# Performance work log

Measured on AMD Instinct MI355X. Metric: run time of the kernel, lower is better.

The kernel has to match this reference:

```python
import jax, jax.numpy as jnp
import numpy as np

DIM = 192
HEADS = 6
HEAD_DIM = DIM // HEADS          # 32
WIN = (4, 4, 4)
SHIFT = (2, 2, 2)
VOL = (64, 64, 64)               # D, H, W
N = WIN[0] * WIN[1] * WIN[2]     # 64 tokens per window
SCALE = HEAD_DIM ** -0.5
EPS = 1e-5


def _rel_pos_index():
    # static (N, N) int index into the relative-position-bias table
    w = WIN
    coords = np.stack(np.meshgrid(np.arange(w[0]), np.arange(w[1]), np.arange(w[2]), indexing='ij'))
    cf = coords.reshape(3, -1)                       # (3, N)
    rel = (cf[:, :, None] - cf[:, None, :]).transpose(1, 2, 0).astype(np.int64)  # (N, N, 3)
    rel[:, :, 0] += w[0] - 1
    rel[:, :, 1] += w[1] - 1
    rel[:, :, 2] += w[2] - 1
    rel[:, :, 0] *= (2 * w[1] - 1) * (2 * w[2] - 1)
    rel[:, :, 1] *= (2 * w[2] - 1)
    return rel.sum(-1)                               # (N, N)

REL_IDX = _rel_pos_index()


def _window_partition(x):
    # (B, D, H, W, C) -> (B*nW, N, C)
    B, D, H, W, C = x.shape
    x = x.reshape(B, D // WIN[0], WIN[0], H // WIN[1], WIN[1], W // WIN[2], WIN[2], C)
    return x.transpose(0, 1, 3, 5, 2, 4, 6, 7).reshape(-1, N, C)


def _window_reverse(windows, B, D, H, W):
    # (B*nW, N, C) -> (B, D, H, W, C)
    C = windows.shape[-1]
    x = windows.reshape(B, D // WIN[0], H // WIN[1], W // WIN[2], WIN[0], WIN[1], WIN[2], C)
    return x.transpose(0, 1, 4, 2, 5, 3, 6, 7).reshape(B, D, H, W, C)


def _layernorm(x, g, b):
    m = jnp.mean(x, axis=-1, keepdims=True)
    v = jnp.var(x, axis=-1, keepdims=True)
    return (x - m) * jax.lax.rsqrt(v + EPS) * g + b


def _compute_shift_mask():
    # Swin3D compute_mask: (nW, N, N) with 0 / -100
    Dp, Hp, Wp = VOL
    img = np.zeros((1, Dp, Hp, Wp, 1), np.float32)
    cnt = 0
    seg = lambda w, s: (slice(0, -w), slice(-w, -s), slice(-s, None))
    for d in seg(WIN[0], SHIFT[0]):
        for h in seg(WIN[1], SHIFT[1]):
            for w in seg(WIN[2], SHIFT[2]):
                img[:, d, h, w, :] = cnt
                cnt += 1
    mw = img.reshape(1, Dp // WIN[0], WIN[0], Hp // WIN[1], WIN[1], Wp // WIN[2], WIN[2], 1)
    mw = mw.transpose(0, 1, 3, 5, 2, 4, 6, 7).reshape(-1, N)   # (nW, N)
    am = mw[:, None, :] - mw[:, :, None]                        # (nW, N, N)
    return np.where(am != 0, np.float32(-100.0), np.float32(0.0))


def setup_inputs() -> dict:
    key = jax.random.key(0)
    ks = jax.random.split(key, 12)
    B = 1
    D, H, W = VOL
    p = lambda k, shape, s=0.02: (jax.random.normal(k, shape, jnp.float32) * s)
    return {
        'x': jax.random.normal(ks[0], (B, D, H, W, DIM), jnp.float32),
        'mask': jnp.asarray(_compute_shift_mask()),
        'norm1_g': jnp.ones((DIM,), jnp.float32),
        'norm1_b': jnp.zeros((DIM,), jnp.float32),
        'qkv_w': p(ks[1], (3 * DIM, DIM)),
        'qkv_b': jnp.zeros((3 * DIM,), jnp.float32),
        'rpb_table': p(ks[2], ((2 * WIN[0] - 1) * (2 * WIN[1] - 1) * (2 * WIN[2] - 1), HEADS)),
        'proj_w': p(ks[3], (DIM, DIM)),
        'proj_b': jnp.zeros((DIM,), jnp.float32),
        'norm2_g': jnp.ones((DIM,), jnp.float32),
        'norm2_b': jnp.zeros((DIM,), jnp.float32),
        'fc1_w': p(ks[4], (4 * DIM, DIM)),
        'fc1_b': jnp.zeros((4 * DIM,), jnp.float32),
        'fc2_w': p(ks[5], (DIM, 4 * DIM)),
        'fc2_b': jnp.zeros((DIM,), jnp.float32),
    }


def reference(x, mask, norm1_g, norm1_b, qkv_w, qkv_b, rpb_table, proj_w, proj_b,
              norm2_g, norm2_b, fc1_w, fc1_b, fc2_w, fc2_b):
    B, D, H, W, C = x.shape
    shortcut = x
    # --- part1: norm1 -> shift -> windowed attention -> unshift ---
    h_ = _layernorm(x, norm1_g, norm1_b)
    h_ = jnp.roll(h_, shift=(-SHIFT[0], -SHIFT[1], -SHIFT[2]), axis=(1, 2, 3))
    xw = _window_partition(h_)                                  # (B*nW, N, C)
    Bn = xw.shape[0]
    qkv = (xw @ qkv_w.T + qkv_b).reshape(Bn, N, 3, HEADS, HEAD_DIM)
    qkv = qkv.transpose(2, 0, 3, 1, 4)                          # (3, Bn, h, N, hd)
    q, k, v = qkv[0] * SCALE, qkv[1], qkv[2]
    attn = jnp.einsum('bhnd,bhmd->bhnm', q, k)                  # (Bn, h, N, N)
    bias = rpb_table[REL_IDX.reshape(-1)].reshape(N, N, HEADS).transpose(2, 0, 1)
    attn = attn + bias[None]
    nW = mask.shape[0]
    attn = attn.reshape(Bn // nW, nW, HEADS, N, N) + mask[None, :, None]
    attn = jax.nn.softmax(attn.reshape(Bn, HEADS, N, N), axis=-1)
    out = jnp.einsum('bhnm,bhmd->bhnd', attn, v).transpose(0, 2, 1, 3).reshape(Bn, N, C)
    out = out @ proj_w.T + proj_b
    h_ = _window_reverse(out, B, D, H, W)
    h_ = jnp.roll(h_, shift=SHIFT, axis=(1, 2, 3))
    x = shortcut + h_                                           # drop_path = identity
    # --- part2: norm2 -> MLP ---
    y = _layernorm(x, norm2_g, norm2_b)
    y = jax.nn.gelu(y @ fc1_w.T + fc1_b, approximate=False) @ fc2_w.T + fc2_b
    return x + y
```

## Files before the change

kernel.cpp:

```cpp
#include <hip/hip_runtime.h>

#define AS1 __attribute__((address_space(1)))
#define AS3 __attribute__((address_space(3)))

typedef short short8 __attribute__((ext_vector_type(8)));
typedef float floatx4 __attribute__((ext_vector_type(4)));

#define NTOK 262144
#define NWIN 4096
#define QKV_SCALE 0.17677669529663687f

__device__ __forceinline__ unsigned short f2bf(float f) {
  unsigned u = __builtin_bit_cast(unsigned, f);
  u += 0x7fffu + ((u >> 16) & 1u);
  return (unsigned short)(u >> 16);
}

__device__ __forceinline__ void gl_lds16(const void* g, void* l) {
  __builtin_amdgcn_global_load_lds((AS1 void*)g, (AS3 void*)l, 16, 0, 0);
}

template <int K>
__device__ __forceinline__ void gemm_core(const unsigned short* __restrict__ A,
                                          const unsigned short* __restrict__ W,
                                          int m0, int n0,
                                          unsigned short* smA, unsigned short* smB,
                                          floatx4 acc[2][4]) {
  const int t = threadIdx.x;
  const int lane = t & 63;
  const int w = t >> 6;
  const int kg = lane >> 4;
  const int l15 = lane & 15;
  const int rA = t >> 2;
  const int q = t & 3;

#pragma unroll
  for (int i = 0; i < 2; i++)
#pragma unroll
    for (int j = 0; j < 4; j++) acc[i][j] = floatx4{0.f, 0.f, 0.f, 0.f};

  for (int k0 = 0; k0 < K; k0 += 32) {
    __syncthreads();
    {
      const int s0 = (q ^ ((rA >> 1) & 3)) << 3;
      gl_lds16(A + (m0 + rA) * K + k0 + s0, (char*)smA + t * 16);
      const int r1 = rA + 64;
      const int s1 = (q ^ ((r1 >> 1) & 3)) << 3;
      gl_lds16(A + (m0 + r1) * K + k0 + s1, (char*)smA + 4096 + t * 16);
      gl_lds16(W + (n0 + rA) * K + k0 + s0, (char*)smB + t * 16);
    }
    asm volatile("s_waitcnt vmcnt(0)" ::: "memory");
    __syncthreads();

    short8 a[2], b[4];
#pragma unroll
    for (int rb = 0; rb < 2; rb++) {
      int row = w * 32 + rb * 16 + l15;
      a[rb] = *(const short8*)((const char*)smA + row * 64 + ((kg ^ ((row >> 1) & 3)) << 4));
    }
#pragma unroll
    for (int cb = 0; cb < 4; cb++) {
      int col = cb * 16 + l15;
      b[cb] = *(const short8*)((const char*)smB + col * 64 + ((kg ^ ((col >> 1) & 3)) << 4));
    }
#pragma unroll
    for (int rb = 0; rb < 2; rb++)
#pragma unroll
      for (int cb = 0; cb < 4; cb++)
        acc[rb][cb] = __builtin_amdgcn_mfma_f32_16x16x32_bf16(a[rb], b[cb], acc[rb][cb], 0, 0, 0);
  }
}

__global__ __launch_bounds__(256) void k_wcvt(const float* __restrict__ src,
                                              unsigned short* __restrict__ dst, int n) {
  int i = blockIdx.x * 256 + threadIdx.x;
  if (i < n) dst[i] = f2bf(src[i]);
}

__global__ __launch_bounds__(256) void k_bias(const float* __restrict__ rpb,
                                              float* __restrict__ btab) {
  int i = blockIdx.x * 256 + threadIdx.x;
  int h = i >> 12, rc = i & 4095, r = rc >> 6, c = rc & 63;
  int dd = (r >> 4) - (c >> 4) + 3;
  int dh = ((r >> 2) & 3) - ((c >> 2) & 3) + 3;
  int dw = (r & 3) - (c & 3) + 3;
  int rel = dd * 49 + dh * 7 + dw;
  btab[i] = rpb[rel * 6 + h];
}

__global__ __launch_bounds__(256) void k_ln1(const float* __restrict__ x,
                                             const float* __restrict__ g,
                                             const float* __restrict__ b,
                                             unsigned short* __restrict__ xw) {
  int w = threadIdx.x >> 6, lane = threadIdx.x & 63;
  int id = blockIdx.x * 4 + w;
  int win = id >> 6, tok = id & 63;
  int bd = win >> 8, bh = (win >> 4) & 15, bw = win & 15;
  int td = tok >> 4, th = (tok >> 2) & 3, tw = tok & 3;
  int sd = (bd * 4 + td + 2) & 63, sh = (bh * 4 + th + 2) & 63, sw = (bw * 4 + tw + 2) & 63;
  const float* row = x + ((sd * 64 + sh) * 64 + sw) * 192;
  float v0 = row[lane], v1 = row[lane + 64], v2 = row[lane + 128];
  float s = v0 + v1 + v2, ss = v0 * v0 + v1 * v1 + v2 * v2;
#pragma unroll
  for (int o = 1; o < 64; o <<= 1) { s += __shfl_xor(s, o); ss += __shfl_xor(ss, o); }
  float mean = s * (1.0f / 192.0f);
  float var = ss * (1.0f / 192.0f) - mean * mean;
  float inv = rsqrtf(var + 1e-5f);
  unsigned short* orow = xw + id * 192;
  orow[lane]       = f2bf((v0 - mean) * inv * g[lane] + b[lane]);
  orow[lane + 64]  = f2bf((v1 - mean) * inv * g[lane + 64] + b[lane + 64]);
  orow[lane + 128] = f2bf((v2 - mean) * inv * g[lane + 128] + b[lane + 128]);
}

__global__ __launch_bounds__(256) void k_ln2(const float* __restrict__ xin,
                                             const float* __restrict__ g,
                                             const float* __restrict__ b,
                                             unsigned short* __restrict__ xn) {
  int w = threadIdx.x >> 6, lane = threadIdx.x & 63;
  int id = blockIdx.x * 4 + w;
  const float* row = xin + id * 192;
  float v0 = row[lane], v1 = row[lane + 64], v2 = row[lane + 128];
  float s = v0 + v1 + v2, ss = v0 * v0 + v1 * v1 + v2 * v2;
#pragma unroll
  for (int o = 1; o < 64; o <<= 1) { s += __shfl_xor(s, o); ss += __shfl_xor(ss, o); }
  float mean = s * (1.0f / 192.0f);
  float var = ss * (1.0f / 192.0f) - mean * mean;
  float inv = rsqrtf(var + 1e-5f);
  unsigned short* orow = xn + id * 192;
  orow[lane]       = f2bf((v0 - mean) * inv * g[lane] + b[lane]);
  orow[lane + 64]  = f2bf((v1 - mean) * inv * g[lane + 64] + b[lane + 64]);
  orow[lane + 128] = f2bf((v2 - mean) * inv * g[lane + 128] + b[lane + 128]);
}

__global__ __launch_bounds__(256) void k_qkv(const unsigned short* __restrict__ xw,
                                             const unsigned short* __restrict__ wq,
                                             const float* __restrict__ qkv_b,
                                             unsigned short* __restrict__ qb,
                                             unsigned short* __restrict__ kb,
                                             unsigned short* __restrict__ vb) {
  __shared__ __attribute__((aligned(16))) unsigned short smA[128 * 32];
  __shared__ __attribute__((aligned(16))) unsigned short smB[64 * 32];
  floatx4 acc[2][4];
  int m0 = blockIdx.x * 128, n0 = blockIdx.y * 64;
  gemm_core<192>(xw, wq, m0, n0, smA, smB, acc);
  int t = threadIdx.x, lane = t & 63, w = t >> 6, kg = lane >> 4, l15 = lane & 15;
#pragma unroll
  for (int rb = 0; rb < 2; rb++)
#pragma unroll
    for (int cb = 0; cb < 4; cb++) {
      int n = n0 + cb * 16 + l15;
      int sel = n / 192, rem = n % 192;
      int head = rem >> 5, d = rem & 31;
      float bias = qkv_b[n];
#pragma unroll
      for (int reg = 0; reg < 4; reg++) {
        int m = m0 + w * 32 + rb * 16 + kg * 4 + reg;
        int win = m >> 6, tok = m & 63;
        float v = acc[rb][cb][reg] + bias;
        if (sel == 0)      qb[((win * 6 + head) * 64 + tok) * 32 + d] = f2bf(v * QKV_SCALE);
        else if (sel == 1) kb[((win * 6 + head) * 64 + tok) * 32 + d] = f2bf(v);
        else               vb[((win * 6 + head) * 32 + d) * 64 + tok] = f2bf(v);
      }
    }
}

__global__ __launch_bounds__(256) void k_proj(const unsigned short* __restrict__ ob,
                                              const unsigned short* __restrict__ wp,
                                              const float* __restrict__ pb,
                                              const float* __restrict__ x,
                                              float* __restrict__ out) {
  __shared__ __attribute__((aligned(16))) unsigned short smA[128 * 32];
  __shared__ __attribute__((aligned(16))) unsigned short smB[64 * 32];
  floatx4 acc[2][4];
  int m0 = blockIdx.x * 128, n0 = blockIdx.y * 64;
  gemm_core<192>(ob, wp, m0, n0, smA, smB, acc);
  int t = threadIdx.x, lane = t & 63, w = t >> 6, kg = lane >> 4, l15 = lane & 15;
#pragma unroll
  for (int rb = 0; rb < 2; rb++)
#pragma unroll
    for (int cb = 0; cb < 4; cb++) {
      int n = n0 + cb * 16 + l15;
      float bias = pb[n];
#pragma unroll
      for (int reg = 0; reg < 4; reg++) {
        int m = m0 + w * 32 + rb * 16 + kg * 4 + reg;
        int win = m >> 6, tok = m & 63;
        int bd = win >> 8, bh = (win >> 4) & 15, bw = win & 15;
        int td = tok >> 4, th = (tok >> 2) & 3, tw = tok & 3;
        int od = (bd * 4 + td + 2) & 63, oh = (bh * 4 + th + 2) & 63, ow = (bw * 4 + tw + 2) & 63;
        int orow = (od * 64 + oh) * 64 + ow;
        out[orow * 192 + n] = x[orow * 192 + n] + acc[rb][cb][reg] + bias;
      }
    }
}

__global__ __launch_bounds__(256) void k_fc1(const unsigned short* __restrict__ xn,
                                             const unsigned short* __restrict__ w1,
                                             const float* __restrict__ b1,
                                             unsigned short* __restrict__ h1, int mbase) {
  __shared__ __attribute__((aligned(16))) unsigned short smA[128 * 32];
  __shared__ __attribute__((aligned(16))) unsigned short smB[64 * 32];
  floatx4 acc[2][4];
  int m0 = mbase + blockIdx.x * 128, n0 = blockIdx.y * 64;
  gemm_core<192>(xn, w1, m0, n0, smA, smB, acc);
  int t = threadIdx.x, lane = t & 63, w = t >> 6, kg = lane >> 4, l15 = lane & 15;
#pragma unroll
  for (int rb = 0; rb < 2; rb++)
#pragma unroll
    for (int cb = 0; cb < 4; cb++) {
      int n = n0 + cb * 16 + l15;
      float bias = b1[n];
#pragma unroll
      for (int reg = 0; reg < 4; reg++) {
        int mr = blockIdx.x * 128 + w * 32 + rb * 16 + kg * 4 + reg;
        float v = acc[rb][cb][reg] + bias;
        float gl = 0.5f * v * (1.0f + erff(v * 0.70710678118654752f));
        h1[mr * 768 + n] = f2bf(gl);
      }
    }
}

__global__ __launch_bounds__(256) void k_fc2(const unsigned short* __restrict__ h1,
                                             const unsigned short* __restrict__ w2,
                                             const float* __restrict__ b2,
                                             float* __restrict__ out, int mbase) {
  __shared__ __attribute__((aligned(16))) unsigned short smA[128 * 32];
  __shared__ __attribute__((aligned(16))) unsigned short smB[64 * 32];
  floatx4 acc[2][4];
  int m0 = blockIdx.x * 128, n0 = blockIdx.y * 64;
  gemm_core<768>(h1, w2, m0, n0, smA, smB, acc);
  int t = threadIdx.x, lane = t & 63, w = t >> 6, kg = lane >> 4, l15 = lane & 15;
#pragma unroll
  for (int rb = 0; rb < 2; rb++)
#pragma unroll
    for (int cb = 0; cb < 4; cb++) {
      int n = n0 + cb * 16 + l15;
      float bias = b2[n];
#pragma unroll
      for (int reg = 0; reg < 4; reg++) {
        int m = mbase + m0 + w * 32 + rb * 16 + kg * 4 + reg;
        out[m * 192 + n] = out[m * 192 + n] + acc[rb][cb][reg] + bias;
      }
    }
}

__global__ __launch_bounds__(384) void k_attn(const unsigned short* __restrict__ qb,
                                              const unsigned short* __restrict__ kb,
                                              const unsigned short* __restrict__ vb,
                                              const float* __restrict__ mask,
                                              const float* __restrict__ btab,
                                              unsigned short* __restrict__ ob) {
  __shared__ __attribute__((aligned(16))) unsigned short P[6][64][72];
  int win = blockIdx.x;
  int h = threadIdx.x >> 6;
  int lane = threadIdx.x & 63;
  int kg = lane >> 4, l15 = lane & 15;

  const short8* Q  = (const short8*)(qb + (win * 6 + h) * 2048);
  const short8* Kf = (const short8*)(kb + (win * 6 + h) * 2048);
  const short8* Vt = (const short8*)(vb + (win * 6 + h) * 2048);

  short8 aQ[4], bK[4];
#pragma unroll
  for (int i = 0; i < 4; i++) aQ[i] = Q[(i * 16 + l15) * 4 + kg];
#pragma unroll
  for (int j = 0; j < 4; j++) bK[j] = Kf[(j * 16 + l15) * 4 + kg];

  floatx4 sc[4][4];
#pragma unroll
  for (int i = 0; i < 4; i++)
#pragma unroll
    for (int j = 0; j < 4; j++) {
      floatx4 z = floatx4{0.f, 0.f, 0.f, 0.f};
      sc[i][j] = __builtin_amdgcn_mfma_f32_16x16x32_bf16(aQ[i], bK[j], z, 0, 0, 0);
    }

  const float* mrow = mask + win * 4096;
  const float* brow = btab + h * 4096;
#pragma unroll
  for (int i = 0; i < 4; i++) {
#pragma unroll
    for (int reg = 0; reg < 4; reg++) {
      int r = i * 16 + kg * 4 + reg;
      float e[4];
      float rm = -1e30f;
#pragma unroll
      for (int j = 0; j < 4; j++) {
        int c = j * 16 + l15;
        float v = sc[i][j][reg] + brow[r * 64 + c] + mrow[r * 64 + c];
        e[j] = v;
        rm = fmaxf(rm, v);
      }
      rm = fmaxf(rm, __shfl_xor(rm, 1));
      rm = fmaxf(rm, __shfl_xor(rm, 2));
      rm = fmaxf(rm, __shfl_xor(rm, 4));
      rm = fmaxf(rm, __shfl_xor(rm, 8));
      float rs = 0.f;
#pragma unroll
      for (int j = 0; j < 4; j++) { e[j] = __expf(e[j] - rm); rs += e[j]; }
      rs += __shfl_xor(rs, 1); rs += __shfl_xor(rs, 2);
      rs += __shfl_xor(rs, 4); rs += __shfl_xor(rs, 8);
      float inv = 1.0f / rs;
#pragma unroll
      for (int j = 0; j < 4; j++) P[h][r][j * 16 + l15] = f2bf(e[j] * inv);
    }
  }
  __syncthreads();

  floatx4 o[4][2];
#pragma unroll
  for (int rb = 0; rb < 4; rb++)
#pragma unroll
    for (int db = 0; db < 2; db++) o[rb][db] = floatx4{0.f, 0.f, 0.f, 0.f};

#pragma unroll
  for (int kk = 0; kk < 2; kk++) {
    short8 pv[4];
#pragma unroll
    for (int rb = 0; rb < 4; rb++)
      pv[rb] = *(const short8*)(&P[h][rb * 16 + l15][kk * 32 + kg * 8]);
#pragma unroll
    for (int db = 0; db < 2; db++) {
      short8 vv = Vt[(db * 16 + l15) * 8 + kk * 4 + kg];
#pragma unroll
      for (int rb = 0; rb < 4; rb++)
        o[rb][db] = __builtin_amdgcn_mfma_f32_16x16x32_bf16(pv[rb], vv, o[rb][db], 0, 0, 0);
    }
  }

#pragma unroll
  for (int rb = 0; rb < 4; rb++)
#pragma unroll
    for (int db = 0; db < 2; db++)
#pragma unroll
      for (int reg = 0; reg < 4; reg++) {
        int tok = rb * 16 + kg * 4 + reg;
        int d = db * 16 + l15;
        ob[(win * 64 + tok) * 192 + h * 32 + d] = f2bf(o[rb][db][reg]);
      }
}

extern "C" void kernel_launch(void* const* d_in, const int* in_sizes, int n_in,
                              void* d_out, int out_size, void* d_ws, size_t ws_size,
                              hipStream_t stream) {
  const float* x     = (const float*)d_in[0];
  const float* mask  = (const float*)d_in[1];
  const float* n1g   = (const float*)d_in[2];
  const float* n1b   = (const float*)d_in[3];
  const float* qkvw  = (const float*)d_in[4];
  const float* qkvb  = (const float*)d_in[5];
  const float* rpb   = (const float*)d_in[6];
  const float* projw = (const float*)d_in[7];
  const float* projb = (const float*)d_in[8];
  const float* n2g   = (const float*)d_in[9];
  const float* n2b   = (const float*)d_in[10];
  const float* fc1w  = (const float*)d_in[11];
  const float* fc1b  = (const float*)d_in[12];
  const float* fc2w  = (const float*)d_in[13];
  const float* fc2b  = (const float*)d_in[14];
  float* out = (float*)d_out;
  char* ws = (char*)d_ws;

  unsigned short* xw = (unsigned short*)(ws);
  unsigned short* qb = (unsigned short*)(ws + 100663296);
  unsigned short* kb = (unsigned short*)(ws + 201326592);
  unsigned short* vb = (unsigned short*)(ws + 301989888);
  unsigned short* h1 = qb;
  unsigned short* wq = (unsigned short*)(ws + 402653184);
  unsigned short* wp = wq + 110592;
  unsigned short* w1 = wp + 36864;
  unsigned short* w2 = w1 + 147456;
  float* btab = (float*)(ws + 402653184 + 884736);

  k_wcvt<<<dim3((110592 + 255) / 256), 256, 0, stream>>>(qkvw, wq, 110592);
  k_wcvt<<<dim3((36864 + 255) / 256), 256, 0, stream>>>(projw, wp, 36864);
  k_wcvt<<<dim3((147456 + 255) / 256), 256, 0, stream>>>(fc1w, w1, 147456);
  k_wcvt<<<dim3((147456 + 255) / 256), 256, 0, stream>>>(fc2w, w2, 147456);
  k_bias<<<dim3(96), 256, 0, stream>>>(rpb, btab);

  k_ln1<<<dim3(65536), 256, 0, stream>>>(x, n1g, n1b, xw);
  k_qkv<<<dim3(2048, 9), 256, 0, stream>>>(xw, wq, qkvb, qb, kb, vb);
  k_attn<<<dim3(4096), 384, 0, stream>>>(qb, kb, vb, mask, btab, xw );
  k_proj<<<dim3(2048, 3), 256, 0, stream>>>(xw, wp, projb, x, out);
  k_ln2<<<dim3(65536), 256, 0, stream>>>(out, n2g, n2b, xw );
  for (int c = 0; c < 4; c++) {
    k_fc1<<<dim3(512, 12), 256, 0, stream>>>(xw, w1, fc1b, h1, c * 65536);
    k_fc2<<<dim3(512, 3), 256, 0, stream>>>(h1, w2, fc2b, out, c * 65536);
  }
}
```

Measured before the change: 1.505 ms.

## Fuse layernorms into GEMMs, stage full-K tiles, compute shift mask analytically

```diff
diff --git a/kernel.cpp b/kernel.cpp
--- a/kernel.cpp
+++ b/kernel.cpp
@@ -4,10 +4,9 @@
 #define AS3 __attribute__((address_space(3)))
 
 typedef short short8 __attribute__((ext_vector_type(8)));
+typedef short short4v __attribute__((ext_vector_type(4)));
 typedef float floatx4 __attribute__((ext_vector_type(4)));
 
-#define NTOK 262144
-#define NWIN 4096
 #define QKV_SCALE 0.17677669529663687f
 
 __device__ __forceinline__ unsigned short f2bf(float f) {
@@ -20,55 +19,21 @@
   __builtin_amdgcn_global_load_lds((AS1 void*)g, (AS3 void*)l, 16, 0, 0);
 }
 
-template <int K>
-__device__ __forceinline__ void gemm_core(const unsigned short* __restrict__ A,
-                                          const unsigned short* __restrict__ W,
-                                          int m0, int n0,
-                                          unsigned short* smA, unsigned short* smB,
-                                          floatx4 acc[2][4]) {
+template <int ITERS>
+__device__ __forceinline__ void stage_tile(const unsigned short* __restrict__ src, int rstride,
+                                           unsigned short* lds) {
   const int t = threadIdx.x;
-  const int lane = t & 63;
-  const int w = t >> 6;
-  const int kg = lane >> 4;
-  const int l15 = lane & 15;
-  const int rA = t >> 2;
-  const int q = t & 3;
-
-#pragma unroll
-  for (int i = 0; i < 2; i++)
-#pragma unroll
-    for (int j = 0; j < 4; j++) acc[i][j] = floatx4{0.f, 0.f, 0.f, 0.f};
-
-  for (int k0 = 0; k0 < K; k0 += 32) {
-    __syncthreads();
-    {
-      const int s0 = (q ^ ((rA >> 1) & 3)) << 3;
-      gl_lds16(A + (m0 + rA) * K + k0 + s0, (char*)smA + t * 16);
-      const int r1 = rA + 64;
-      const int s1 = (q ^ ((r1 >> 1) & 3)) << 3;
-      gl_lds16(A + (m0 + r1) * K + k0 + s1, (char*)smA + 4096 + t * 16);
-      gl_lds16(W + (n0 + rA) * K + k0 + s0, (char*)smB + t * 16);
-    }
-    asm volatile("s_waitcnt vmcnt(0)" ::: "memory");
-    __syncthreads();
-
-    short8 a[2], b[4];
-#pragma unroll
-    for (int rb = 0; rb < 2; rb++) {
-      int row = w * 32 + rb * 16 + l15;
-      a[rb] = *(const short8*)((const char*)smA + row * 64 + ((kg ^ ((row >> 1) & 3)) << 4));
-    }
-#pragma unroll
-    for (int cb = 0; cb < 4; cb++) {
-      int col = cb * 16 + l15;
-      b[cb] = *(const short8*)((const char*)smB + col * 64 + ((kg ^ ((col >> 1) & 3)) << 4));
-    }
-#pragma unroll
-    for (int rb = 0; rb < 2; rb++)
-#pragma unroll
-      for (int cb = 0; cb < 4; cb++)
-        acc[rb][cb] = __builtin_amdgcn_mfma_f32_16x16x32_bf16(a[rb], b[cb], acc[rb][cb], 0, 0, 0);
-  }
+#pragma unroll
+  for (int i = 0; i < ITERS; i++) {
+    int D = i * 256 + t;
+    int row = D / 24, sl = D - row * 24;
+    int ss = sl ^ (row & 7);
+    gl_lds16(src + row * rstride + ss * 8, (char*)lds + D * 16);
+  }
+}
+
+__device__ __forceinline__ short8 frag192(const unsigned short* lds, int row, int ks, int kg) {
+  return *(const short8*)((const char*)lds + row * 384 + ((((ks << 2) + kg) ^ (row & 7)) << 4));
 }
 
 __global__ __launch_bounds__(256) void k_wcvt(const float* __restrict__ src,
@@ -84,170 +49,128 @@
   int dd = (r >> 4) - (c >> 4) + 3;
   int dh = ((r >> 2) & 3) - ((c >> 2) & 3) + 3;
   int dw = (r & 3) - (c & 3) + 3;
-  int rel = dd * 49 + dh * 7 + dw;
-  btab[i] = rpb[rel * 6 + h];
-}
-
-__global__ __launch_bounds__(256) void k_ln1(const float* __restrict__ x,
-                                             const float* __restrict__ g,
-                                             const float* __restrict__ b,
-                                             unsigned short* __restrict__ xw) {
-  int w = threadIdx.x >> 6, lane = threadIdx.x & 63;
-  int id = blockIdx.x * 4 + w;
-  int win = id >> 6, tok = id & 63;
-  int bd = win >> 8, bh = (win >> 4) & 15, bw = win & 15;
-  int td = tok >> 4, th = (tok >> 2) & 3, tw = tok & 3;
-  int sd = (bd * 4 + td + 2) & 63, sh = (bh * 4 + th + 2) & 63, sw = (bw * 4 + tw + 2) & 63;
-  const float* row = x + ((sd * 64 + sh) * 64 + sw) * 192;
-  float v0 = row[lane], v1 = row[lane + 64], v2 = row[lane + 128];
-  float s = v0 + v1 + v2, ss = v0 * v0 + v1 * v1 + v2 * v2;
-#pragma unroll
-  for (int o = 1; o < 64; o <<= 1) { s += __shfl_xor(s, o); ss += __shfl_xor(ss, o); }
-  float mean = s * (1.0f / 192.0f);
-  float var = ss * (1.0f / 192.0f) - mean * mean;
-  float inv = rsqrtf(var + 1e-5f);
-  unsigned short* orow = xw + id * 192;
-  orow[lane]       = f2bf((v0 - mean) * inv * g[lane] + b[lane]);
-  orow[lane + 64]  = f2bf((v1 - mean) * inv * g[lane + 64] + b[lane + 64]);
-  orow[lane + 128] = f2bf((v2 - mean) * inv * g[lane + 128] + b[lane + 128]);
-}
-
-__global__ __launch_bounds__(256) void k_ln2(const float* __restrict__ xin,
-                                             const float* __restrict__ g,
-                                             const float* __restrict__ b,
-                                             unsigned short* __restrict__ xn) {
-  int w = threadIdx.x >> 6, lane = threadIdx.x & 63;
-  int id = blockIdx.x * 4 + w;
-  const float* row = xin + id * 192;
-  float v0 = row[lane], v1 = row[lane + 64], v2 = row[lane + 128];
-  float s = v0 + v1 + v2, ss = v0 * v0 + v1 * v1 + v2 * v2;
-#pragma unroll
-  for (int o = 1; o < 64; o <<= 1) { s += __shfl_xor(s, o); ss += __shfl_xor(ss, o); }
-  float mean = s * (1.0f / 192.0f);
-  float var = ss * (1.0f / 192.0f) - mean * mean;
-  float inv = rsqrtf(var + 1e-5f);
-  unsigned short* orow = xn + id * 192;
-  orow[lane]       = f2bf((v0 - mean) * inv * g[lane] + b[lane]);
-  orow[lane + 64]  = f2bf((v1 - mean) * inv * g[lane + 64] + b[lane + 64]);
-  orow[lane + 128] = f2bf((v2 - mean) * inv * g[lane + 128] + b[lane + 128]);
-}
-
-__global__ __launch_bounds__(256) void k_qkv(const unsigned short* __restrict__ xw,
-                                             const unsigned short* __restrict__ wq,
-                                             const float* __restrict__ qkv_b,
-                                             unsigned short* __restrict__ qb,
-                                             unsigned short* __restrict__ kb,
-                                             unsigned short* __restrict__ vb) {
-  __shared__ __attribute__((aligned(16))) unsigned short smA[128 * 32];
-  __shared__ __attribute__((aligned(16))) unsigned short smB[64 * 32];
+  btab[i] = rpb[(dd * 49 + dh * 7 + dw) * 6 + h];
+}
+
+__global__ __launch_bounds__(256, 2) void k_qkv(const float* __restrict__ x,
+                                                const float* __restrict__ g,
+                                                const float* __restrict__ bb,
+                                                const unsigned short* __restrict__ wq,
+                                                const float* __restrict__ qkv_b,
+                                                unsigned short* __restrict__ qb,
+                                                unsigned short* __restrict__ kb,
+                                                unsigned short* __restrict__ vb) {
+  __shared__ __attribute__((aligned(16))) unsigned short smA[128 * 192];
+  __shared__ __attribute__((aligned(16))) unsigned short smB[64 * 192];
+  const int t = threadIdx.x;
+  const int m0 = blockIdx.x * 128;
+
+  {
+    int r = t >> 1, half = t & 1;
+    int id = m0 + r, win = id >> 6, tok = id & 63;
+    int bd = win >> 8, bh = (win >> 4) & 15, bw = win & 15;
+    int sd = ((bd << 2) + (tok >> 4) + 2) & 63;
+    int sh = ((bh << 2) + ((tok >> 2) & 3) + 2) & 63;
+    int sw = ((bw << 2) + (tok & 3) + 2) & 63;
+    const float4* rp = (const float4*)(x + ((sd * 64 + sh) * 64 + sw) * 192 + half * 96);
+    float4 v[24];
+#pragma unroll
+    for (int j = 0; j < 24; j++) v[j] = rp[j];
+    float s = 0.f, ss = 0.f;
+#pragma unroll
+    for (int j = 0; j < 24; j++) {
+      s += v[j].x + v[j].y + v[j].z + v[j].w;
+      ss += v[j].x * v[j].x + v[j].y * v[j].y + v[j].z * v[j].z + v[j].w * v[j].w;
+    }
+    s += __shfl_xor(s, 1);
+    ss += __shfl_xor(ss, 1);
+    float mean = s * (1.0f / 192.0f);
+    float inv = rsqrtf(ss * (1.0f / 192.0f) - mean * mean + 1e-5f);
+    const float4* gp = (const float4*)(g + half * 96);
+    const float4* bp = (const float4*)(bb + half * 96);
+#pragma unroll
+    for (int j = 0; j < 12; j++) {
+      float4 a0 = v[2 * j], a1 = v[2 * j + 1];
+      float4 g0 = gp[2 * j], g1 = gp[2 * j + 1];
+      float4 c0 = bp[2 * j], c1 = bp[2 * j + 1];
+      short8 o;
+      o[0] = (short)f2bf((a0.x - mean) * inv * g0.x + c0.x);
+      o[1] = (short)f2bf((a0.y - mean) * inv * g0.y + c0.y);
+      o[2] = (short)f2bf((a0.z - mean) * inv * g0.z + c0.z);
+      o[3] = (short)f2bf((a0.w - mean) * inv * g0.w + c0.w);
+      o[4] = (short)f2bf((a1.x - mean) * inv * g1.x + c1.x);
+      o[5] = (short)f2bf((a1.y - mean) * inv * g1.y + c1.y);
+      o[6] = (short)f2bf((a1.z - mean) * inv * g1.z + c1.z);
+      o[7] = (short)f2bf((a1.w - mean) * inv * g1.w + c1.w);
+      int sl = half * 12 + j;
+      *(short8*)((char*)smA + r * 384 + ((sl ^ (r & 7)) << 4)) = o;
+    }
+  }
+
+  const int lane = t & 63, w = t >> 6, kg = lane >> 4, l15 = lane & 15;
+  short8 afr[2][6];
   floatx4 acc[2][4];
-  int m0 = blockIdx.x * 128, n0 = blockIdx.y * 64;
-  gemm_core<192>(xw, wq, m0, n0, smA, smB, acc);
-  int t = threadIdx.x, lane = t & 63, w = t >> 6, kg = lane >> 4, l15 = lane & 15;
-#pragma unroll
-  for (int rb = 0; rb < 2; rb++)
+
+  for (int c = 0; c < 9; c++) {
+    if (c) __syncthreads();
+    stage_tile<6>(wq + c * 64 * 192, 192, smB);
+    asm volatile("s_waitcnt vmcnt(0)" ::: "memory");
+    __syncthreads();
+    if (c == 0) {
+#pragma unroll
+      for (int rb = 0; rb < 2; rb++)
+#pragma unroll
+        for (int ks = 0; ks < 6; ks++)
+          afr[rb][ks] = frag192(smA, w * 32 + rb * 16 + l15, ks, kg);
+    }
+#pragma unroll
+    for (int rb = 0; rb < 2; rb++)
+#pragma unroll
+      for (int cb = 0; cb < 4; cb++) acc[rb][cb] = floatx4{0.f, 0.f, 0.f, 0.f};
+#pragma unroll
+    for (int ks = 0; ks < 6; ks++) {
+      short8 b[4];
+#pragma unroll
+      for (int cb = 0; cb < 4; cb++) b[cb] = frag192(smB, cb * 16 + l15, ks, kg);
+#pragma unroll
+      for (int rb = 0; rb < 2; rb++)
+#pragma unroll
+        for (int cb = 0; cb < 4; cb++)
+          acc[rb][cb] = __builtin_amdgcn_mfma_f32_16x16x32_bf16(afr[rb][ks], b[cb], acc[rb][cb], 0, 0, 0);
+    }
 #pragma unroll
     for (int cb = 0; cb < 4; cb++) {
-      int n = n0 + cb * 16 + l15;
-      int sel = n / 192, rem = n % 192;
+      int n = c * 64 + cb * 16 + l15;
+      int sel = n / 192, rem = n - sel * 192;
       int head = rem >> 5, d = rem & 31;
       float bias = qkv_b[n];
 #pragma unroll
-      for (int reg = 0; reg < 4; reg++) {
-        int m = m0 + w * 32 + rb * 16 + kg * 4 + reg;
-        int win = m >> 6, tok = m & 63;
-        float v = acc[rb][cb][reg] + bias;
-        if (sel == 0)      qb[((win * 6 + head) * 64 + tok) * 32 + d] = f2bf(v * QKV_SCALE);
-        else if (sel == 1) kb[((win * 6 + head) * 64 + tok) * 32 + d] = f2bf(v);
-        else               vb[((win * 6 + head) * 32 + d) * 64 + tok] = f2bf(v);
-      }
-    }
-}
-
-__global__ __launch_bounds__(256) void k_proj(const unsigned short* __restrict__ ob,
-                                              const unsigned short* __restrict__ wp,
-                                              const float* __restrict__ pb,
-                                              const float* __restrict__ x,
-                                              float* __restrict__ out) {
-  __shared__ __attribute__((aligned(16))) unsigned short smA[128 * 32];
-  __shared__ __attribute__((aligned(16))) unsigned short smB[64 * 32];
-  floatx4 acc[2][4];
-  int m0 = blockIdx.x * 128, n0 = blockIdx.y * 64;
-  gemm_core<192>(ob, wp, m0, n0, smA, smB, acc);
-  int t = threadIdx.x, lane = t & 63, w = t >> 6, kg = lane >> 4, l15 = lane & 15;
-#pragma unroll
-  for (int rb = 0; rb < 2; rb++)
-#pragma unroll
-    for (int cb = 0; cb < 4; cb++) {
-      int n = n0 + cb * 16 + l15;
-      float bias = pb[n];
-#pragma unroll
-      for (int reg = 0; reg < 4; reg++) {
-        int m = m0 + w * 32 + rb * 16 + kg * 4 + reg;
-        int win = m >> 6, tok = m & 63;
-        int bd = win >> 8, bh = (win >> 4) & 15, bw = win & 15;
-        int td = tok >> 4, th = (tok >> 2) & 3, tw = tok & 3;
-        int od = (bd * 4 + td + 2) & 63, oh = (bh * 4 + th + 2) & 63, ow = (bw * 4 + tw + 2) & 63;
-        int orow = (od * 64 + oh) * 64 + ow;
-        out[orow * 192 + n] = x[orow * 192 + n] + acc[rb][cb][reg] + bias;
-      }
-    }
-}
-
-__global__ __launch_bounds__(256) void k_fc1(const unsigned short* __restrict__ xn,
-                                             const unsigned short* __restrict__ w1,
-                                             const float* __restrict__ b1,
-                                             unsigned short* __restrict__ h1, int mbase) {
-  __shared__ __attribute__((aligned(16))) unsigned short smA[128 * 32];
-  __shared__ __attribute__((aligned(16))) unsigned short smB[64 * 32];
-  floatx4 acc[2][4];
-  int m0 = mbase + blockIdx.x * 128, n0 = blockIdx.y * 64;
-  gemm_core<192>(xn, w1, m0, n0, smA, smB, acc);
-  int t = threadIdx.x, lane = t & 63, w = t >> 6, kg = lane >> 4, l15 = lane & 15;
-#pragma unroll
-  for (int rb = 0; rb < 2; rb++)
-#pragma unroll
-    for (int cb = 0; cb < 4; cb++) {
-      int n = n0 + cb * 16 + l15;
-      float bias = b1[n];
-#pragma unroll
-      for (int reg = 0; reg < 4; reg++) {
-        int mr = blockIdx.x * 128 + w * 32 + rb * 16 + kg * 4 + reg;
-        float v = acc[rb][cb][reg] + bias;
-        float gl = 0.5f * v * (1.0f + erff(v * 0.70710678118654752f));
-        h1[mr * 768 + n] = f2bf(gl);
-      }
-    }
-}
-
-__global__ __launch_bounds__(256) void k_fc2(const unsigned short* __restrict__ h1,
-                                             const unsigned short* __restrict__ w2,
-                                             const float* __restrict__ b2,
-                                             float* __restrict__ out, int mbase) {
-  __shared__ __attribute__((aligned(16))) unsigned short smA[128 * 32];
-  __shared__ __attribute__((aligned(16))) unsigned short smB[64 * 32];
-  floatx4 acc[2][4];
-  int m0 = blockIdx.x * 128, n0 = blockIdx.y * 64;
-  gemm_core<768>(h1, w2, m0, n0, smA, smB, acc);
-  int t = threadIdx.x, lane = t & 63, w = t >> 6, kg = lane >> 4, l15 = lane & 15;
-#pragma unroll
-  for (int rb = 0; rb < 2; rb++)
-#pragma unroll
-    for (int cb = 0; cb < 4; cb++) {
-      int n = n0 + cb * 16 + l15;
-      float bias = b2[n];
-#pragma unroll
-      for (int reg = 0; reg < 4; reg++) {
-        int m = mbase + m0 + w * 32 + rb * 16 + kg * 4 + reg;
-        out[m * 192 + n] = out[m * 192 + n] + acc[rb][cb][reg] + bias;
-      }
-    }
+      for (int rb = 0; rb < 2; rb++) {
+        int mb = m0 + w * 32 + rb * 16 + kg * 4;
+        int win = mb >> 6, tk0 = mb & 63;
+        if (sel == 2) {
+          short4v pk;
+#pragma unroll
+          for (int reg = 0; reg < 4; reg++) pk[reg] = (short)f2bf(acc[rb][cb][reg] + bias);
+          *(short4v*)(vb + ((win * 6 + head) * 32 + d) * 64 + tk0) = pk;
+        } else {
+#pragma unroll
+          for (int reg = 0; reg < 4; reg++) {
+            float v = acc[rb][cb][reg] + bias;
+            if (sel == 0)
+              qb[((win * 6 + head) * 64 + tk0 + reg) * 32 + d] = f2bf(v * QKV_SCALE);
+            else
+              kb[((win * 6 + head) * 64 + tk0 + reg) * 32 + d] = f2bf(v);
+          }
+        }
+      }
+    }
+  }
 }
 
 __global__ __launch_bounds__(384) void k_attn(const unsigned short* __restrict__ qb,
                                               const unsigned short* __restrict__ kb,
                                               const unsigned short* __restrict__ vb,
-                                              const float* __restrict__ mask,
                                               const float* __restrict__ btab,
                                               unsigned short* __restrict__ ob) {
   __shared__ __attribute__((aligned(16))) unsigned short P[6][64][72];
@@ -256,7 +179,10 @@
   int lane = threadIdx.x & 63;
   int kg = lane >> 4, l15 = lane & 15;
 
-  const short8* Q  = (const short8*)(qb + (win * 6 + h) * 2048);
+  int mm = (((win >> 8) == 15) ? 32 : 0) | ((((win >> 4) & 15) == 15) ? 8 : 0) |
+           (((win & 15) == 15) ? 2 : 0);
+
+  const short8* Q = (const short8*)(qb + (win * 6 + h) * 2048);
   const short8* Kf = (const short8*)(kb + (win * 6 + h) * 2048);
   const short8* Vt = (const short8*)(vb + (win * 6 + h) * 2048);
 
@@ -275,7 +201,6 @@
       sc[i][j] = __builtin_amdgcn_mfma_f32_16x16x32_bf16(aQ[i], bK[j], z, 0, 0, 0);
     }
 
-  const float* mrow = mask + win * 4096;
   const float* brow = btab + h * 4096;
 #pragma unroll
   for (int i = 0; i < 4; i++) {
@@ -286,8 +211,9 @@
       float rm = -1e30f;
 #pragma unroll
       for (int j = 0; j < 4; j++) {
-        int c = j * 16 + l15;
-        float v = sc[i][j][reg] + brow[r * 64 + c] + mrow[r * 64 + c];
+        int cidx = j * 16 + l15;
+        float mval = ((r ^ cidx) & mm) ? -100.0f : 0.0f;
+        float v = sc[i][j][reg] + brow[r * 64 + cidx] + mval;
         e[j] = v;
         rm = fmaxf(rm, v);
       }
@@ -340,11 +266,211 @@
       }
 }
 
+__global__ __launch_bounds__(256, 2) void k_proj(const unsigned short* __restrict__ ob,
+                                                 const unsigned short* __restrict__ wp,
+                                                 const float* __restrict__ pb,
+                                                 const float* __restrict__ x,
+                                                 const float* __restrict__ n2g,
+                                                 const float* __restrict__ n2b,
+                                                 float* __restrict__ out,
+                                                 unsigned short* __restrict__ xn) {
+  __shared__ __attribute__((aligned(16))) unsigned short smA[128 * 192];
+  __shared__ __attribute__((aligned(16))) unsigned short smB[64 * 192];
+  const int t = threadIdx.x;
+  const int m0 = blockIdx.x * 128;
+  const int lane = t & 63, w = t >> 6, kg = lane >> 4, l15 = lane & 15;
+
+  stage_tile<12>(ob + m0 * 192, 192, smA);
+
+  floatx4 acc[2][12];
+#pragma unroll
+  for (int rb = 0; rb < 2; rb++)
+#pragma unroll
+    for (int cb = 0; cb < 12; cb++) acc[rb][cb] = floatx4{0.f, 0.f, 0.f, 0.f};
+
+  for (int c = 0; c < 3; c++) {
+    if (c) __syncthreads();
+    stage_tile<6>(wp + c * 64 * 192, 192, smB);
+    asm volatile("s_waitcnt vmcnt(0)" ::: "memory");
+    __syncthreads();
+#pragma unroll
+    for (int ks = 0; ks < 6; ks++) {
+      short8 a[2], b[4];
+#pragma unroll
+      for (int rb = 0; rb < 2; rb++) a[rb] = frag192(smA, w * 32 + rb * 16 + l15, ks, kg);
+#pragma unroll
+      for (int cb = 0; cb < 4; cb++) b[cb] = frag192(smB, cb * 16 + l15, ks, kg);
+#pragma unroll
+      for (int rb = 0; rb < 2; rb++)
+#pragma unroll
+        for (int cb = 0; cb < 4; cb++)
+          acc[rb][c * 4 + cb] =
+              __builtin_amdgcn_mfma_f32_16x16x32_bf16(a[rb], b[cb], acc[rb][c * 4 + cb], 0, 0, 0);
+    }
+  }
+
+  float bias[12], gg[12], bv[12];
+#pragma unroll
+  for (int cb = 0; cb < 12; cb++) {
+    int n = cb * 16 + l15;
+    bias[cb] = pb[n];
+    gg[cb] = n2g[n];
+    bv[cb] = n2b[n];
+  }
+#pragma unroll
+  for (int rb = 0; rb < 2; rb++)
+#pragma unroll
+    for (int reg = 0; reg < 4; reg++) {
+      int m = m0 + w * 32 + rb * 16 + kg * 4 + reg;
+      int win = m >> 6, tok = m & 63;
+      int bd = win >> 8, bh = (win >> 4) & 15, bw = win & 15;
+      int od = ((bd << 2) + (tok >> 4) + 2) & 63;
+      int oh = ((bh << 2) + ((tok >> 2) & 3) + 2) & 63;
+      int ow = ((bw << 2) + (tok & 3) + 2) & 63;
+      int orow = (od * 64 + oh) * 64 + ow;
+      const float* xr = x + orow * 192;
+      float* orp = out + orow * 192;
+      unsigned short* xnp = xn + orow * 192;
+      float s = 0.f, ss = 0.f;
+#pragma unroll
+      for (int cb = 0; cb < 12; cb++) {
+        float v = acc[rb][cb][reg] + bias[cb] + xr[cb * 16 + l15];
+        acc[rb][cb][reg] = v;
+        s += v;
+        ss += v * v;
+      }
+      s += __shfl_xor(s, 1); ss += __shfl_xor(ss, 1);
+      s += __shfl_xor(s, 2); ss += __shfl_xor(ss, 2);
+      s += __shfl_xor(s, 4); ss += __shfl_xor(ss, 4);
+      s += __shfl_xor(s, 8); ss += __shfl_xor(ss, 8);
+      float mean = s * (1.0f / 192.0f);
+      float inv = rsqrtf(ss * (1.0f / 192.0f) - mean * mean + 1e-5f);
+#pragma unroll
+      for (int cb = 0; cb < 12; cb++) {
+        float v = acc[rb][cb][reg];
+        orp[cb * 16 + l15] = v;
+        xnp[cb * 16 + l15] = f2bf((v - mean) * inv * gg[cb] + bv[cb]);
+      }
+    }
+}
+
+__global__ __launch_bounds__(256, 2) void k_fc1(const unsigned short* __restrict__ xn,
+                                                const unsigned short* __restrict__ w1,
+                                                const float* __restrict__ b1,
+                                                unsigned short* __restrict__ h1, int mbase) {
+  __shared__ __attribute__((aligned(16))) unsigned short smA[128 * 192];
+  __shared__ __attribute__((aligned(16))) unsigned short smB[64 * 192];
+  const int t = threadIdx.x;
+  const int mr0 = blockIdx.x * 128;
+  const int lane = t & 63, w = t >> 6, kg = lane >> 4, l15 = lane & 15;
+
+  stage_tile<12>(xn + (mbase + mr0) * 192, 192, smA);
+
+  short8 afr[2][6];
+  floatx4 acc[2][4];
+  for (int c = 0; c < 12; c++) {
+    if (c) __syncthreads();
+    stage_tile<6>(w1 + c * 64 * 192, 192, smB);
+    asm volatile("s_waitcnt vmcnt(0)" ::: "memory");
+    __syncthreads();
+    if (c == 0) {
+#pragma unroll
+      for (int rb = 0; rb < 2; rb++)
+#pragma unroll
+        for (int ks = 0; ks < 6; ks++)
+          afr[rb][ks] = frag192(smA, w * 32 + rb * 16 + l15, ks, kg);
+    }
+#pragma unroll
+    for (int rb = 0; rb < 2; rb++)
+#pragma unroll
+      for (int cb = 0; cb < 4; cb++) acc[rb][cb] = floatx4{0.f, 0.f, 0.f, 0.f};
+#pragma unroll
+    for (int ks = 0; ks < 6; ks++) {
+      short8 b[4];
+#pragma unroll
+      for (int cb = 0; cb < 4; cb++) b[cb] = frag192(smB, cb * 16 + l15, ks, kg);
+#pragma unroll
+      for (int rb = 0; rb < 2; rb++)
+#pragma unroll
+        for (int cb = 0; cb < 4; cb++)
+          acc[rb][cb] = __builtin_amdgcn_mfma_f32_16x16x32_bf16(afr[rb][ks], b[cb], acc[rb][cb], 0, 0, 0);
+    }
+#pragma unroll
+    for (int cb = 0; cb < 4; cb++) {
+      int n = c * 64 + cb * 16 + l15;
+      float bias = b1[n];
+#pragma unroll
+      for (int rb = 0; rb < 2; rb++)
+#pragma unroll
+        for (int reg = 0; reg < 4; reg++) {
+          int mr = mr0 + w * 32 + rb * 16 + kg * 4 + reg;
+          float v = acc[rb][cb][reg] + bias;
+          float gl = 0.5f * v * (1.0f + erff(v * 0.70710678118654752f));
+          h1[mr * 768 + n] = f2bf(gl);
+        }
+    }
+  }
+}
+
+__global__ __launch_bounds__(256, 2) void k_fc2(const unsigned short* __restrict__ h1,
+                                                const unsigned short* __restrict__ w2,
+                                                const float* __restrict__ b2,
+                                                float* __restrict__ out, int mbase) {
+  __shared__ __attribute__((aligned(16))) unsigned short smA[128 * 192];
+  __shared__ __attribute__((aligned(16))) unsigned short smB[64 * 192];
+  const int t = threadIdx.x;
+  const int mr0 = blockIdx.x * 128;
+  const int lane = t & 63, w = t >> 6, kg = lane >> 4, l15 = lane & 15;
+
+  floatx4 acc[2][12];
+#pragma unroll
+  for (int rb = 0; rb < 2; rb++)
+#pragma unroll
+    for (int cb = 0; cb < 12; cb++) acc[rb][cb] = floatx4{0.f, 0.f, 0.f, 0.f};
+
+  for (int p = 0; p < 4; p++) {
+    __syncthreads();
+    stage_tile<12>(h1 + mr0 * 768 + p * 192, 768, smA);
+    for (int c = 0; c < 3; c++) {
+      if (c) __syncthreads();
+      stage_tile<6>(w2 + c * 64 * 768 + p * 192, 768, smB);
+      asm volatile("s_waitcnt vmcnt(0)" ::: "memory");
+      __syncthreads();
+#pragma unroll
+      for (int ks = 0; ks < 6; ks++) {
+        short8 a[2], b[4];
+#pragma unroll
+        for (int rb = 0; rb < 2; rb++) a[rb] = frag192(smA, w * 32 + rb * 16 + l15, ks, kg);
+#pragma unroll
+        for (int cb = 0; cb < 4; cb++) b[cb] = frag192(smB, cb * 16 + l15, ks, kg);
+#pragma unroll
+        for (int rb = 0; rb < 2; rb++)
+#pragma unroll
+          for (int cb = 0; cb < 4; cb++)
+            acc[rb][c * 4 + cb] =
+                __builtin_amdgcn_mfma_f32_16x16x32_bf16(a[rb], b[cb], acc[rb][c * 4 + cb], 0, 0, 0);
+      }
+    }
+  }
+
+#pragma unroll
+  for (int cb = 0; cb < 12; cb++) {
+    int n = cb * 16 + l15;
+    float bias = b2[n];
+#pragma unroll
+    for (int rb = 0; rb < 2; rb++)
+#pragma unroll
+      for (int reg = 0; reg < 4; reg++) {
+        int m = mbase + mr0 + w * 32 + rb * 16 + kg * 4 + reg;
+        out[m * 192 + n] = out[m * 192 + n] + acc[rb][cb][reg] + bias;
+      }
+  }
+}
+
 extern "C" void kernel_launch(void* const* d_in, const int* in_sizes, int n_in,
                               void* d_out, int out_size, void* d_ws, size_t ws_size,
                               hipStream_t stream) {
   const float* x     = (const float*)d_in[0];
-  const float* mask  = (const float*)d_in[1];
   const float* n1g   = (const float*)d_in[2];
   const float* n1b   = (const float*)d_in[3];
   const float* qkvw  = (const float*)d_in[4];
@@ -361,30 +487,29 @@
   float* out = (float*)d_out;
   char* ws = (char*)d_ws;
 
-  unsigned short* xw = (unsigned short*)(ws);
+  unsigned short* ob = (unsigned short*)(ws);
   unsigned short* qb = (unsigned short*)(ws + 100663296);
   unsigned short* kb = (unsigned short*)(ws + 201326592);
   unsigned short* vb = (unsigned short*)(ws + 301989888);
   unsigned short* h1 = qb;
+  unsigned short* xn = kb;
   unsigned short* wq = (unsigned short*)(ws + 402653184);
   unsigned short* wp = wq + 110592;
   unsigned short* w1 = wp + 36864;
   unsigned short* w2 = w1 + 147456;
   float* btab = (float*)(ws + 402653184 + 884736);
 
-  k_wcvt<<<dim3((110592 + 255) / 256), 256, 0, stream>>>(qkvw, wq, 110592);
-  k_wcvt<<<dim3((36864 + 255) / 256), 256, 0, stream>>>(projw, wp, 36864);
-  k_wcvt<<<dim3((147456 + 255) / 256), 256, 0, stream>>>(fc1w, w1, 147456);
-  k_wcvt<<<dim3((147456 + 255) / 256), 256, 0, stream>>>(fc2w, w2, 147456);
+  k_wcvt<<<dim3(432), 256, 0, stream>>>(qkvw, wq, 110592);
+  k_wcvt<<<dim3(144), 256, 0, stream>>>(projw, wp, 36864);
+  k_wcvt<<<dim3(576), 256, 0, stream>>>(fc1w, w1, 147456);
+  k_wcvt<<<dim3(576), 256, 0, stream>>>(fc2w, w2, 147456);
   k_bias<<<dim3(96), 256, 0, stream>>>(rpb, btab);
 
-  k_ln1<<<dim3(65536), 256, 0, stream>>>(x, n1g, n1b, xw);
-  k_qkv<<<dim3(2048, 9), 256, 0, stream>>>(xw, wq, qkvb, qb, kb, vb);
-  k_attn<<<dim3(4096), 384, 0, stream>>>(qb, kb, vb, mask, btab, xw );
-  k_proj<<<dim3(2048, 3), 256, 0, stream>>>(xw, wp, projb, x, out);
-  k_ln2<<<dim3(65536), 256, 0, stream>>>(out, n2g, n2b, xw );
+  k_qkv<<<dim3(2048), 256, 0, stream>>>(x, n1g, n1b, wq, qkvb, qb, kb, vb);
+  k_attn<<<dim3(4096), 384, 0, stream>>>(qb, kb, vb, btab, ob);
+  k_proj<<<dim3(2048), 256, 0, stream>>>(ob, wp, projb, x, n2g, n2b, out, xn);
   for (int c = 0; c < 4; c++) {
-    k_fc1<<<dim3(512, 12), 256, 0, stream>>>(xw, w1, fc1b, h1, c * 65536);
-    k_fc2<<<dim3(512, 3), 256, 0, stream>>>(h1, w2, fc2b, out, c * 65536);
-  }
-}
+    k_fc1<<<dim3(512), 256, 0, stream>>>(xn, w1, fc1b, h1, c * 65536);
+    k_fc2<<<dim3(512), 256, 0, stream>>>(h1, w2, fc2b, out, c * 65536);
+  }
+}
```

Measured after the change: 1.290 ms. 1.17x faster.
